# Optimization experiments

Hardware: AMD Instinct MI355X
Metric: run time of the kernel (lower is better)

Reference implementation:

```python
import jax, jax.numpy as jnp
import numpy as np

D_MODEL, D_HIDDEN, N_EXPERTS = 1024, 4096, 8
CAP_FACTOR, LBL_COEF, ZLOSS_COEF = 1.25, 0.01, 0.0


def setup_inputs() -> dict:
    key = jax.random.key(0)
    ks = jax.random.split(key, 4)
    B, T = 4, 2048
    x = jax.random.normal(ks[0], (B, T, D_MODEL), dtype=jnp.float32)
    # router linear
    Wr = jax.random.normal(ks[1], (D_MODEL, N_EXPERTS), jnp.float32) / np.sqrt(D_MODEL).astype(np.float32)
    br = jnp.zeros((N_EXPERTS,), jnp.float32)
    # per-expert MLP: fc1 [D->H], gelu, fc2 [H->D]
    W1 = jax.random.normal(ks[2], (N_EXPERTS, D_MODEL, D_HIDDEN), jnp.float32) / np.sqrt(D_MODEL).astype(np.float32)
    b1 = jnp.zeros((N_EXPERTS, D_HIDDEN), jnp.float32)
    W2 = jax.random.normal(ks[3], (N_EXPERTS, D_HIDDEN, D_MODEL), jnp.float32) / np.sqrt(D_HIDDEN).astype(np.float32)
    b2 = jnp.zeros((N_EXPERTS, D_MODEL), jnp.float32)
    return {"x": x, "Wr": Wr, "br": br, "W1": W1, "b1": b1, "W2": W2, "b2": b2}


def reference(x, Wr, br, W1, b1, W2, b2):
    B, T, D = x.shape
    N = B * T
    E = Wr.shape[1]
    cap = int(CAP_FACTOR * (N / E) + 1)  # static Python int

    h = x.reshape(N, D)
    # --- Top1Router ---
    logits = h @ Wr + br                              # [N, E]
    probs = jax.nn.softmax(logits, axis=-1)
    top1 = jnp.argmax(probs, axis=-1)                 # [N]
    w = jnp.take_along_axis(probs, top1[:, None], axis=1)  # [N, 1]
    assign = jax.nn.one_hot(top1, E, dtype=jnp.float32)    # constant wrt grads
    importance = probs.mean(axis=0)
    load = jax.lax.stop_gradient(assign).mean(axis=0)
    lb_loss = E * jnp.sum(importance * load)
    z_loss = jnp.mean(jax.nn.logsumexp(logits, axis=-1) ** 2)

    # --- capacity-based dispatch (first `cap` tokens per expert, token order) ---
    pos = (jnp.cumsum(assign, axis=0) * assign).sum(axis=-1).astype(jnp.int32) - 1  # [N] slot within expert
    keep = pos < cap
    slot = jnp.where(keep, pos, cap)  # dropped tokens -> overflow slot `cap`
    xe = jnp.zeros((E, cap + 1, D), x.dtype).at[top1, slot].set(h)[:, :cap]  # [E, cap, D]

    # --- per-expert MLP as grouped GEMMs ---
    he = jax.nn.gelu(jnp.einsum('ecd,edh->ech', xe, W1) + b1[:, None, :])    # [E, cap, H]
    ye = jnp.einsum('ech,ehd->ecd', he, W2) + b2[:, None, :]                 # [E, cap, D]

    # --- combine (gather back, scale by router weight, zero dropped) ---
    out = ye[top1, jnp.minimum(pos, cap - 1)] * w   # [N, D]
    out = jnp.where(keep[:, None], out, jnp.zeros((), x.dtype))
    y = out.reshape(B, T, D)
    aux = LBL_COEF * lb_loss + ZLOSS_COEF * z_loss
    return (y, aux)
```

## Files before the change

kernel.cpp:

```cpp
#include <hip/hip_runtime.h>
#include <hip/hip_bf16.h>

#define N_TOK 8192
#define DM    1024
#define DH    4096
#define NE    8
#define CAP   1281
#define CAPR  1408
#define ISTR  1536

typedef unsigned short u16;
typedef __attribute__((ext_vector_type(8))) __bf16 bf16x8;
typedef __attribute__((ext_vector_type(8))) short short8;
typedef __attribute__((ext_vector_type(4))) short s16x4;
typedef __attribute__((ext_vector_type(4))) float f4;

__device__ __forceinline__ u16 f2bf(float f){
  union { float f; unsigned u; } v; v.f = f;
  unsigned r = v.u + 0x7fffu + ((v.u >> 16) & 1u);
  return (u16)(r >> 16);
}

__device__ __forceinline__ float gelu_fast(float v){
  float u = 0.7978845608028654f * (v + 0.044715f * v * v * v);
  return v * __builtin_amdgcn_rcpf(1.0f + __expf(-2.0f * u));
}

__device__ __forceinline__ void gl2lds16(const void* g, void* l){
  __builtin_amdgcn_global_load_lds((const __attribute__((address_space(1))) void*)g,
                                   (__attribute__((address_space(3))) void*)l, 16, 0, 0);
}

__global__ __launch_bounds__(256) void tcvt_k(const float* __restrict__ in, u16* __restrict__ out,
                                              int K, int Nn){
  __shared__ float tile[64][68];
  size_t mb = (size_t)blockIdx.z * (size_t)K * (size_t)Nn;
  const float* ip = in + mb;
  u16* op = out + mb;
  int n0 = blockIdx.x*64, k0 = blockIdx.y*64;
  int t = threadIdx.x;
  int kr = t>>4, nc = (t&15)*4;
  #pragma unroll
  for (int ii=0;ii<4;ii++){
    f4 v = *(const f4*)&ip[(size_t)(k0+kr+16*ii)*Nn + n0 + nc];
    tile[kr+16*ii][nc+0] = v[0]; tile[kr+16*ii][nc+1] = v[1];
    tile[kr+16*ii][nc+2] = v[2]; tile[kr+16*ii][nc+3] = v[3];
  }
  __syncthreads();
  int nr = t>>2, kc = (t&3)*16;
  short8 o0, o1;
  #pragma unroll
  for (int c=0;c<8;c++){
    o0[c] = (short)f2bf(tile[kc+c][nr]);
    o1[c] = (short)f2bf(tile[kc+8+c][nr]);
  }
  *(short8*)&op[(size_t)(n0+nr)*K + k0 + kc] = o0;
  *(short8*)&op[(size_t)(n0+nr)*K + k0 + kc + 8] = o1;
}

__global__ __launch_bounds__(256) void router_k(const float* __restrict__ x, const float* __restrict__ Wr,
    const float* __restrict__ br, u16* __restrict__ Xb, int* __restrict__ top1,
    float* __restrict__ wgt, float* __restrict__ impSum){
  __shared__ float pSh[4][8];
  int wid = threadIdx.x >> 6, lane = threadIdx.x & 63;
  int n = blockIdx.x * 4 + wid;
  const float* xr = x + (size_t)n * DM;
  u16* xbr = Xb + (size_t)n * DM;
  float acc[8];
  #pragma unroll
  for (int e=0;e<8;e++) acc[e]=0.f;
  #pragma unroll
  for (int c=0;c<4;c++){
    int d0 = c*256 + lane*4;
    f4 xv = *(const f4*)(xr + d0);
    s16x4 xb;
    #pragma unroll
    for (int j=0;j<4;j++) xb[j] = (short)f2bf(xv[j]);
    *(s16x4*)(xbr + d0) = xb;
    #pragma unroll
    for (int j=0;j<4;j++){
      const float* wrow = Wr + (size_t)(d0+j)*NE;
      float xs = xv[j];
      #pragma unroll
      for (int e=0;e<8;e++) acc[e] = fmaf(xs, wrow[e], acc[e]);
    }
  }
  #pragma unroll
  for (int off=32; off>0; off>>=1){
    #pragma unroll
    for (int e=0;e<8;e++) acc[e] += __shfl_down(acc[e], off, 64);
  }
  if (lane==0){
    float lg[8]; float mx = -1e30f;
    #pragma unroll
    for (int e=0;e<8;e++){ lg[e] = acc[e] + br[e]; mx = fmaxf(mx, lg[e]); }
    float p[8], s=0.f;
    #pragma unroll
    for (int e=0;e<8;e++){ p[e] = expf(lg[e]-mx); s += p[e]; }
    int bt=0; float bv=lg[0];
    #pragma unroll
    for (int e=1;e<8;e++){ if (lg[e]>bv){ bv=lg[e]; bt=e; } }
    float inv = 1.f/s;
    top1[n] = bt; wgt[n] = p[bt]*inv;
    #pragma unroll
    for (int e=0;e<8;e++) pSh[wid][e] = p[e]*inv;
  }
  __syncthreads();
  if (threadIdx.x < 8){
    int e = threadIdx.x;
    atomicAdd(&impSum[e], pSh[0][e]+pSh[1][e]+pSh[2][e]+pSh[3][e]);
  }
}

__global__ __launch_bounds__(1024) void scan_k(const int* __restrict__ top1, int* __restrict__ idx,
    int* __restrict__ cnt, int* __restrict__ dropList, int* __restrict__ nDrop,
    const float* __restrict__ impSum, float* __restrict__ auxOut){
  __shared__ int waveCnt[16][8];
  __shared__ int wavePre[16][8];
  __shared__ int chunkTot[8];
  __shared__ int base_s[8];
  int tid = threadIdx.x, wid = tid>>6, lane = tid&63;
  if (tid < 8) base_s[tid] = 0;
  __syncthreads();
  for (int c=0;c<8;c++){
    int t = c*1024 + tid;
    int e = top1[t];
    int myPre = 0;
    #pragma unroll
    for (int ex=0; ex<8; ex++){
      unsigned long long mk = __ballot(e == ex);
      if (lane == 0) waveCnt[wid][ex] = __popcll(mk);
      if (ex == e) myPre = __popcll(mk & ((1ull<<lane)-1ull));
    }
    __syncthreads();
    if (tid < 8){
      int run = 0;
      for (int wv=0; wv<16; wv++){ wavePre[wv][tid] = run; run += waveCnt[wv][tid]; }
      chunkTot[tid] = run;
    }
    __syncthreads();
    int pos = base_s[e] + wavePre[wid][e] + myPre;
    if (pos < CAP) idx[e*ISTR + pos] = t;
    else { int d = atomicAdd(nDrop, 1); dropList[d] = t; }
    __syncthreads();
    if (tid < 8) base_s[tid] += chunkTot[tid];
    __syncthreads();
  }
  if (tid < 8){
    cnt[tid] = base_s[tid] < CAP ? base_s[tid] : CAP;
  }
  if (tid == 0){
    float s = 0.f;
    for (int e=0;e<8;e++) s += (impSum[e]*(1.f/N_TOK)) * ((float)base_s[e]*(1.f/N_TOK));
    *auxOut = 0.01f * 8.f * s;
  }
}

__global__ __launch_bounds__(256) void zdrop_k(const int* __restrict__ dropList,
    const int* __restrict__ nDrop, float* __restrict__ y){
  int nd = *nDrop;
  for (int i = blockIdx.x; i < nd; i += gridDim.x){
    int t = dropList[i];
    f4* row = (f4*)(y + (size_t)t * DM);
    f4 z; z[0]=0.f; z[1]=0.f; z[2]=0.f; z[3]=0.f;
    row[threadIdx.x] = z;
  }
}


#define LDA(buf, m, kk) (*(const bf16x8*)&lds[(buf)*16384 + (aBase ^ ((kk)*32)) + (m)*1024])
#define LDB(buf, n, kk) (*(const bf16x8*)&lds[32768 + (buf)*16384 + (bBase ^ ((kk)*32)) + (n)*1024])

#define SA_J(buf, j, kc) gl2lds16(aS[j] + (size_t)(kc)*64, &lds[(buf)*16384 + ((j)*512 + t)*8])
#define SB_ALLM(buf, kc) do{ \
  gl2lds16(bS[0] + (size_t)(kc)*64, &lds[32768 + (buf)*16384 + (0*512 + t)*8]); \
  gl2lds16(bS[1] + (size_t)(kc)*64, &lds[32768 + (buf)*16384 + (1*512 + t)*8]); \
  gl2lds16(bS[2] + (size_t)(kc)*64, &lds[32768 + (buf)*16384 + (2*512 + t)*8]); \
  gl2lds16(bS[3] + (size_t)(kc)*64, &lds[32768 + (buf)*16384 + (3*512 + t)*8]); }while(0)

#define SB0 __builtin_amdgcn_sched_barrier(0)
#define LGKM(n) do{ asm volatile("s_waitcnt lgkmcnt(" #n ")" ::: "memory"); SB0; }while(0)

#define READ_A(dst, mbase, buf) do{ \
  dst[0][0]=LDA(buf,(mbase),0);   dst[0][1]=LDA(buf,(mbase),1); \
  dst[1][0]=LDA(buf,(mbase)+1,0); dst[1][1]=LDA(buf,(mbase)+1,1); }while(0)

#define MFMA_PAIR(q, A_) \
  _Pragma("unroll") for (int j_=0;j_<2;j_++) \
    _Pragma("unroll") for (int n_=0;n_<4;n_++) \
      _Pragma("unroll") for (int kk_=0;kk_<2;kk_++) \
        acc[2*(q)+j_][n_] = __builtin_amdgcn_mfma_f32_16x16x32_bf16(A_[j_][kk_], Bf[n_][kk_], acc[2*(q)+j_][n_], 0,0,0);

#define KTILE(buf, ktv, NTv) do{ \
  int kc1 = (ktv)+1 < (NTv) ? (ktv)+1 : (NTv)-1; \
  int kc2 = (ktv)+2 < (NTv) ? (ktv)+2 : (NTv)-1; \
   \
  asm volatile("s_waitcnt vmcnt(6)" ::: "memory"); \
  __builtin_amdgcn_s_barrier(); \
  SA_J((buf)^1, 1, kc1); SA_J((buf)^1, 3, kc1); \
  _Pragma("unroll") for (int n_=0;n_<4;n_++){ Bf[n_][0] = LDB(buf,n_,0); Bf[n_][1] = LDB(buf,n_,1); } \
  READ_A(aA, 0, buf); \
  SB0;  \
  READ_A(aB, 2, buf); \
  LGKM(4);   \
  __builtin_amdgcn_s_setprio(1); MFMA_PAIR(0, aA); __builtin_amdgcn_s_setprio(0); \
   \
  __builtin_amdgcn_s_barrier(); \
  SB_ALLM(buf, kc2); \
  READ_A(aA, 4, buf); \
  LGKM(4);   \
  __builtin_amdgcn_s_setprio(1); MFMA_PAIR(1, aB); __builtin_amdgcn_s_setprio(0); \
   \
  __builtin_amdgcn_s_barrier(); \
  SA_J(buf, 0, kc2); SA_J(buf, 2, kc2); \
  READ_A(aB, 6, buf); \
  LGKM(4);   \
  __builtin_amdgcn_s_setprio(1); MFMA_PAIR(2, aA); __builtin_amdgcn_s_setprio(0); \
   \
  __builtin_amdgcn_s_barrier(); \
  LGKM(0);   \
  __builtin_amdgcn_s_setprio(1); MFMA_PAIR(3, aB); __builtin_amdgcn_s_setprio(0); \
}while(0)

#define GEMM_PROLOGUE() do{ \
  SB_ALLM(0, 0); \
  SA_J(0,0,0); SA_J(0,2,0); \
  SA_J(0,1,0); SA_J(0,3,0); \
  SB_ALLM(1, 1); \
  SA_J(1,0,1); SA_J(1,2,1); }while(0)

__global__ __launch_bounds__(512, 2) void gemm1_k(
    const u16* __restrict__ Xb, const u16* __restrict__ W1T,
    const float* __restrict__ b1, const int* __restrict__ idx,
    const int* __restrict__ cnt, u16* __restrict__ He)
{
  int bid = blockIdx.x;
  int x = bid & 7, k = bid >> 3;
  int g = x*16 + k/6;
  int ntS = k - (k/6)*6;
  int e = g >> 4, mtH = g & 15;
  int cn = cnt[e];
  if (ntS*256 >= cn) return;
  __shared__ __align__(16) u16 lds[65536];
  int t = threadIdx.x, lane = t&63, wid = t>>6;
  int waveM = wid>>2, waveN = wid&3;
  int rA = lane&15, kb = lane>>4, s = rA&7;

  const u16* aS[4]; const u16* bS[4];
  #pragma unroll
  for (int j=0;j<4;j++){
    int pos = j*512 + t;
    int row = pos>>3, ch = pos&7;
    int gcb = ch ^ (row&7);
    aS[j] = W1T + ((size_t)e*DH + mtH*256 + row)*DM + gcb*8;
    int slotrow = ntS*256 + row;
    int token = (slotrow < cn) ? idx[e*ISTR + slotrow] : 0;
    bS[j] = Xb + (size_t)token*DM + gcb*8;
  }
  f4 acc[8][4];
  #pragma unroll
  for (int m=0;m<8;m++)
    #pragma unroll
    for (int n=0;n<4;n++)
      #pragma unroll
      for (int j=0;j<4;j++) acc[m][n][j]=0.f;

  int aBase = (waveM*128 + rA)*64 + (kb ^ s)*8;
  int bBase = (waveN*64  + rA)*64 + (kb ^ s)*8;
  bf16x8 Bf[4][2], aA[2][2], aB[2][2];

  GEMM_PROLOGUE();
  const int NT = DM/64;
  #pragma unroll 1
  for (int i=0;i<NT/2;i++){
    KTILE(0, 2*i,   NT);
    KTILE(1, 2*i+1, NT);
  }
  asm volatile("s_waitcnt vmcnt(0) lgkmcnt(0)" ::: "memory");

  int rG = lane>>4;
  #pragma unroll
  for (int m=0;m<8;m++){
    int h0 = mtH*256 + waveM*128 + m*16 + rG*4;
    f4 b4 = *(const f4*)&b1[e*DH + h0];
    #pragma unroll
    for (int n=0;n<4;n++){
      int slot = ntS*256 + waveN*64 + n*16 + rA;
      if (slot < cn){
        s16x4 v;
        #pragma unroll
        for (int j=0;j<4;j++) v[j] = (short)f2bf(gelu_fast(acc[m][n][j] + b4[j]));
        *(s16x4*)&He[((size_t)e*CAPR + slot)*DH + h0] = v;
      }
    }
  }
}

__global__ __launch_bounds__(512, 2) void gemm2_k(
    const u16* __restrict__ He, const u16* __restrict__ W2T,
    const float* __restrict__ b2, const int* __restrict__ idx,
    const int* __restrict__ cnt, const float* __restrict__ wgt,
    float* __restrict__ y)
{
  int bid = blockIdx.x;
  int x = bid & 7, k = bid >> 3;
  int g = x*4 + k/6;
  int mt = k - (k/6)*6;
  int e = g >> 2, nt = g & 3;
  int cn = cnt[e];
  if (mt*256 >= cn) return;
  __shared__ __align__(16) u16 lds[65536];
  int t = threadIdx.x, lane = t&63, wid = t>>6;
  int waveM = wid>>2, waveN = wid&3;
  int rA = lane&15, kb = lane>>4, s = rA&7;

  const u16* aS[4]; const u16* bS[4];
  #pragma unroll
  for (int j=0;j<4;j++){
    int pos = j*512 + t;
    int row = pos>>3, ch = pos&7;
    int gcb = ch ^ (row&7);
    int srow = mt*256 + row; if (srow >= cn) srow = cn-1;
    aS[j] = He  + ((size_t)e*CAPR + srow)*DH + gcb*8;
    bS[j] = W2T + ((size_t)e*DM + nt*256 + row)*DH + gcb*8;
  }
  f4 acc[8][4];
  #pragma unroll
  for (int m=0;m<8;m++)
    #pragma unroll
    for (int n=0;n<4;n++)
      #pragma unroll
      for (int j=0;j<4;j++) acc[m][n][j]=0.f;

  int aBase = (waveM*128 + rA)*64 + (kb ^ s)*8;
  int bBase = (waveN*64  + rA)*64 + (kb ^ s)*8;
  bf16x8 Bf[4][2], aA[2][2], aB[2][2];

  GEMM_PROLOGUE();
  const int NT = DH/64;
  #pragma unroll 1
  for (int i=0;i<NT/2;i++){
    KTILE(0, 2*i,   NT);
    KTILE(1, 2*i+1, NT);
  }
  asm volatile("s_waitcnt vmcnt(0) lgkmcnt(0)" ::: "memory");

  int rG = lane>>4;
  float bias_[4];
  #pragma unroll
  for (int n=0;n<4;n++) bias_[n] = b2[e*DM + nt*256 + waveN*64 + n*16 + rA];
  #pragma unroll
  for (int m=0;m<8;m++){
    int slot0 = mt*256 + waveM*128 + m*16 + rG*4;
    #pragma unroll
    for (int j=0;j<4;j++){
      int slot = slot0 + j;
      bool valid = slot < cn;
      int tk = valid ? idx[e*ISTR + slot] : 0;
      float wv = valid ? wgt[tk] : 0.f;
      float* yr = y + (size_t)tk*DM;
      #pragma unroll
      for (int n=0;n<4;n++){
        int col = nt*256 + waveN*64 + n*16 + rA;
        if (valid) yr[col] = (acc[m][n][j] + bias_[n]) * wv;
      }
    }
  }
}

extern "C" void kernel_launch(void* const* d_in, const int* in_sizes, int n_in,
                              void* d_out, int out_size, void* d_ws, size_t ws_size,
                              hipStream_t stream){
  const float* x  = (const float*)d_in[0];
  const float* Wr = (const float*)d_in[1];
  const float* br = (const float*)d_in[2];
  const float* W1 = (const float*)d_in[3];
  const float* b1 = (const float*)d_in[4];
  const float* W2 = (const float*)d_in[5];
  const float* b2 = (const float*)d_in[6];
  float* y = (float*)d_out;

  char* ws = (char*)d_ws;
  u16* Xb  = (u16*)(ws);
  u16* W1T = (u16*)(ws + 16777216ull);
  u16* W2T = (u16*)(ws + 16777216ull + 67108864ull);
  u16* He  = (u16*)(ws + 16777216ull + 2ull*67108864ull);
  char* tail = ws + 16777216ull + 2ull*67108864ull + (size_t)NE*CAPR*DH*2ull;
  int*   top1   = (int*)(tail);
  float* wgt    = (float*)(tail + 32768);
  int*   idx    = (int*)(tail + 65536);
  int*   drop   = (int*)(tail + 65536 + 49152);
  float* impSum = (float*)(tail + 65536 + 49152 + 32768);
  int*   nDrop  = (int*)((char*)impSum + 32);
  int*   cnt    = nDrop + 1;

  (void)hipMemsetAsync(impSum, 0, 64, stream);

  tcvt_k<<<dim3(64,16,8), 256, 0, stream>>>(W1, W1T, DM, DH);
  tcvt_k<<<dim3(16,64,8), 256, 0, stream>>>(W2, W2T, DH, DM);
  router_k<<<2048, 256, 0, stream>>>(x, Wr, br, Xb, top1, wgt, impSum);
  scan_k<<<1, 1024, 0, stream>>>(top1, idx, cnt, drop, nDrop, impSum,
                                 y + (size_t)N_TOK*DM);
  zdrop_k<<<64, 256, 0, stream>>>(drop, nDrop, y);
  gemm1_k<<<768, 512, 0, stream>>>(Xb, W1T, b1, idx, cnt, He);
  gemm2_k<<<192, 512, 0, stream>>>(He, W2T, b2, idx, cnt, wgt, y);

  (void)in_sizes; (void)n_in; (void)out_size; (void)ws_size;
}
```

Measured before the change: 347.4 us.

## Retile gemm2 to 128x128 tiles with 256-thread blocks for more parallelism

Rewrites the second grouped GEMM from 256x256 tiles with 512 threads (192 blocks) to 128x128 tiles with 256 threads (704 blocks), with a new half-size K-tile pipeline and LDS layout. The aim is to fix under-occupancy: 192 blocks cannot fill the CUs of an MI355X, and with capacity 1281 per expert, mt=5 blocks were mostly padding. In exchange, the smaller tiles give lower arithmetic intensity per block, more global loads of W2 and He, and a simpler schedule with full lgkm waits.

```diff
diff --git a/kernel.cpp b/kernel.cpp
--- a/kernel.cpp
+++ b/kernel.cpp
@@ -167,7 +167,6 @@
   }
 }
 
-
 #define LDA(buf, m, kk) (*(const bf16x8*)&lds[(buf)*16384 + (aBase ^ ((kk)*32)) + (m)*1024])
 #define LDB(buf, n, kk) (*(const bf16x8*)&lds[32768 + (buf)*16384 + (bBase ^ ((kk)*32)) + (n)*1024])
 
@@ -194,31 +193,27 @@
 #define KTILE(buf, ktv, NTv) do{ \
   int kc1 = (ktv)+1 < (NTv) ? (ktv)+1 : (NTv)-1; \
   int kc2 = (ktv)+2 < (NTv) ? (ktv)+2 : (NTv)-1; \
-   \
   asm volatile("s_waitcnt vmcnt(6)" ::: "memory"); \
   __builtin_amdgcn_s_barrier(); \
   SA_J((buf)^1, 1, kc1); SA_J((buf)^1, 3, kc1); \
   _Pragma("unroll") for (int n_=0;n_<4;n_++){ Bf[n_][0] = LDB(buf,n_,0); Bf[n_][1] = LDB(buf,n_,1); } \
   READ_A(aA, 0, buf); \
-  SB0;  \
+  SB0; \
   READ_A(aB, 2, buf); \
-  LGKM(4);   \
+  LGKM(4); \
   __builtin_amdgcn_s_setprio(1); MFMA_PAIR(0, aA); __builtin_amdgcn_s_setprio(0); \
-   \
   __builtin_amdgcn_s_barrier(); \
   SB_ALLM(buf, kc2); \
   READ_A(aA, 4, buf); \
-  LGKM(4);   \
+  LGKM(4); \
   __builtin_amdgcn_s_setprio(1); MFMA_PAIR(1, aB); __builtin_amdgcn_s_setprio(0); \
-   \
   __builtin_amdgcn_s_barrier(); \
   SA_J(buf, 0, kc2); SA_J(buf, 2, kc2); \
   READ_A(aB, 6, buf); \
-  LGKM(4);   \
+  LGKM(4); \
   __builtin_amdgcn_s_setprio(1); MFMA_PAIR(2, aA); __builtin_amdgcn_s_setprio(0); \
-   \
-  __builtin_amdgcn_s_barrier(); \
-  LGKM(0);   \
+  __builtin_amdgcn_s_barrier(); \
+  LGKM(0); \
   __builtin_amdgcn_s_setprio(1); MFMA_PAIR(3, aB); __builtin_amdgcn_s_setprio(0); \
 }while(0)
 
@@ -296,7 +291,55 @@
   }
 }
 
-__global__ __launch_bounds__(512, 2) void gemm2_k(
+#define LDA_H(buf, m, kk) (*(const bf16x8*)&lds[(buf)*8192 + (aBase ^ ((kk)*32)) + (m)*1024])
+#define LDB_H(buf, n, kk) (*(const bf16x8*)&lds[16384 + (buf)*8192 + (bBase ^ ((kk)*32)) + (n)*1024])
+
+#define SA_JH(buf, j, kc) gl2lds16(aS[j] + (size_t)(kc)*64, &lds[(buf)*8192 + ((j)*256 + t)*8])
+#define SB_ALLH(buf, kc) do{ \
+  gl2lds16(bS[0] + (size_t)(kc)*64, &lds[16384 + (buf)*8192 + (0*256 + t)*8]); \
+  gl2lds16(bS[1] + (size_t)(kc)*64, &lds[16384 + (buf)*8192 + (1*256 + t)*8]); \
+  gl2lds16(bS[2] + (size_t)(kc)*64, &lds[16384 + (buf)*8192 + (2*256 + t)*8]); \
+  gl2lds16(bS[3] + (size_t)(kc)*64, &lds[16384 + (buf)*8192 + (3*256 + t)*8]); }while(0)
+
+#define MFMA8_H(mi, AF) \
+  _Pragma("unroll") for (int n_=0;n_<4;n_++) \
+    _Pragma("unroll") for (int kk_=0;kk_<2;kk_++) \
+      acc[(mi)][n_] = __builtin_amdgcn_mfma_f32_16x16x32_bf16(AF[kk_], Bf[n_][kk_], acc[(mi)][n_], 0,0,0);
+
+#define KTILE_H(buf, ktv, NTv) do{ \
+  int kc1 = (ktv)+1 < (NTv) ? (ktv)+1 : (NTv)-1; \
+  int kc2 = (ktv)+2 < (NTv) ? (ktv)+2 : (NTv)-1; \
+   \
+  asm volatile("s_waitcnt vmcnt(6)" ::: "memory"); \
+  __builtin_amdgcn_s_barrier(); \
+  SA_JH((buf)^1, 1, kc1); SA_JH((buf)^1, 3, kc1); \
+  _Pragma("unroll") for (int n_=0;n_<4;n_++){ Bf[n_][0] = LDB_H(buf,n_,0); Bf[n_][1] = LDB_H(buf,n_,1); } \
+  aA[0]=LDA_H(buf,0,0); aA[1]=LDA_H(buf,0,1); \
+  aB[0]=LDA_H(buf,1,0); aB[1]=LDA_H(buf,1,1); \
+  LGKM(0); \
+  __builtin_amdgcn_s_setprio(1); MFMA8_H(0, aA); __builtin_amdgcn_s_setprio(0); \
+   \
+  __builtin_amdgcn_s_barrier(); \
+  SB_ALLH(buf, kc2); \
+  __builtin_amdgcn_s_setprio(1); MFMA8_H(1, aB); __builtin_amdgcn_s_setprio(0); \
+   \
+  aA[0]=LDA_H(buf,2,0); aA[1]=LDA_H(buf,2,1); \
+  aB[0]=LDA_H(buf,3,0); aB[1]=LDA_H(buf,3,1); \
+  SA_JH(buf, 0, kc2); SA_JH(buf, 2, kc2); \
+  LGKM(0); \
+  __builtin_amdgcn_s_setprio(1); MFMA8_H(2, aA); __builtin_amdgcn_s_setprio(0); \
+   \
+  __builtin_amdgcn_s_setprio(1); MFMA8_H(3, aB); __builtin_amdgcn_s_setprio(0); \
+}while(0)
+
+#define GEMM_PROLOGUE_H() do{ \
+  SB_ALLH(0, 0); \
+  SA_JH(0,0,0); SA_JH(0,2,0); \
+  SA_JH(0,1,0); SA_JH(0,3,0); \
+  SB_ALLH(1, 1); \
+  SA_JH(1,0,1); SA_JH(1,2,1); }while(0)
+
+__global__ __launch_bounds__(256, 2) void gemm2_k(
     const u16* __restrict__ He, const u16* __restrict__ W2T,
     const float* __restrict__ b2, const int* __restrict__ idx,
     const int* __restrict__ cnt, const float* __restrict__ wgt,
@@ -304,54 +347,55 @@
 {
   int bid = blockIdx.x;
   int x = bid & 7, k = bid >> 3;
-  int g = x*4 + k/6;
-  int mt = k - (k/6)*6;
-  int e = g >> 2, nt = g & 3;
+  int gi = k / 11;
+  int mt = k - gi*11;
+  int g = x*8 + gi;
+  int e = g >> 3, nt = g & 7;
   int cn = cnt[e];
-  if (mt*256 >= cn) return;
-  __shared__ __align__(16) u16 lds[65536];
+  if (mt*128 >= cn) return;
+  __shared__ __align__(16) u16 lds[32768];
   int t = threadIdx.x, lane = t&63, wid = t>>6;
-  int waveM = wid>>2, waveN = wid&3;
+  int waveM = wid>>1, waveN = wid&1;
   int rA = lane&15, kb = lane>>4, s = rA&7;
 
   const u16* aS[4]; const u16* bS[4];
   #pragma unroll
   for (int j=0;j<4;j++){
-    int pos = j*512 + t;
+    int pos = j*256 + t;
     int row = pos>>3, ch = pos&7;
     int gcb = ch ^ (row&7);
-    int srow = mt*256 + row; if (srow >= cn) srow = cn-1;
+    int srow = mt*128 + row; if (srow >= cn) srow = cn-1;
     aS[j] = He  + ((size_t)e*CAPR + srow)*DH + gcb*8;
-    bS[j] = W2T + ((size_t)e*DM + nt*256 + row)*DH + gcb*8;
-  }
-  f4 acc[8][4];
-  #pragma unroll
-  for (int m=0;m<8;m++)
+    bS[j] = W2T + ((size_t)e*DM + nt*128 + row)*DH + gcb*8;
+  }
+  f4 acc[4][4];
+  #pragma unroll
+  for (int m=0;m<4;m++)
     #pragma unroll
     for (int n=0;n<4;n++)
       #pragma unroll
       for (int j=0;j<4;j++) acc[m][n][j]=0.f;
 
-  int aBase = (waveM*128 + rA)*64 + (kb ^ s)*8;
-  int bBase = (waveN*64  + rA)*64 + (kb ^ s)*8;
-  bf16x8 Bf[4][2], aA[2][2], aB[2][2];
-
-  GEMM_PROLOGUE();
+  int aBase = (waveM*64 + rA)*64 + (kb ^ s)*8;
+  int bBase = (waveN*64 + rA)*64 + (kb ^ s)*8;
+  bf16x8 Bf[4][2], aA[2], aB[2];
+
+  GEMM_PROLOGUE_H();
   const int NT = DH/64;
   #pragma unroll 1
   for (int i=0;i<NT/2;i++){
-    KTILE(0, 2*i,   NT);
-    KTILE(1, 2*i+1, NT);
+    KTILE_H(0, 2*i,   NT);
+    KTILE_H(1, 2*i+1, NT);
   }
   asm volatile("s_waitcnt vmcnt(0) lgkmcnt(0)" ::: "memory");
 
   int rG = lane>>4;
   float bias_[4];
   #pragma unroll
-  for (int n=0;n<4;n++) bias_[n] = b2[e*DM + nt*256 + waveN*64 + n*16 + rA];
-  #pragma unroll
-  for (int m=0;m<8;m++){
-    int slot0 = mt*256 + waveM*128 + m*16 + rG*4;
+  for (int n=0;n<4;n++) bias_[n] = b2[e*DM + nt*128 + waveN*64 + n*16 + rA];
+  #pragma unroll
+  for (int m=0;m<4;m++){
+    int slot0 = mt*128 + waveM*64 + m*16 + rG*4;
     #pragma unroll
     for (int j=0;j<4;j++){
       int slot = slot0 + j;
@@ -361,7 +405,7 @@
       float* yr = y + (size_t)tk*DM;
       #pragma unroll
       for (int n=0;n<4;n++){
-        int col = nt*256 + waveN*64 + n*16 + rA;
+        int col = nt*128 + waveN*64 + n*16 + rA;
         if (valid) yr[col] = (acc[m][n][j] + bias_[n]) * wv;
       }
     }
@@ -403,7 +447,7 @@
                                  y + (size_t)N_TOK*DM);
   zdrop_k<<<64, 256, 0, stream>>>(drop, nDrop, y);
   gemm1_k<<<768, 512, 0, stream>>>(Xb, W1T, b1, idx, cnt, He);
-  gemm2_k<<<192, 512, 0, stream>>>(He, W2T, b2, idx, cnt, wgt, y);
+  gemm2_k<<<704, 256, 0, stream>>>(He, W2T, b2, idx, cnt, wgt, y);
 
   (void)in_sizes; (void)n_in; (void)out_size; (void)ws_size;
 }
```

Result: slower. 364.5 us (+4.9%).
